# Kernel tuning notes

Measured on AMD Instinct MI355X. Metric: run time of the kernel, lower is better.

Reference implementation:

```python
import jax, jax.numpy as jnp
import numpy as np

B, S, H, GRID = 8, 4096, 1152, 64  # 64x64 patch grid, pooled 4x4 -> 256


def setup_inputs() -> dict:
    key = jax.random.key(0)
    k1, = jax.random.split(key, 1)
    hidden_states = jax.random.normal(k1, (B, S, H), dtype=jnp.float32)
    idx = jnp.arange(S, dtype=jnp.int32)
    pos = jnp.stack([idx % GRID, idx // GRID], axis=-1)  # (S,2) = (x,y)
    pixel_position_ids = jnp.broadcast_to(pos, (B, S, 2))
    padding_positions = jnp.zeros((B, S), dtype=bool)
    return {
        "hidden_states": hidden_states,
        "pixel_position_ids": pixel_position_ids,
        "padding_positions": padding_positions,
        "output_length": 256,
    }


def reference(hidden_states, pixel_position_ids, padding_positions, output_length):
    # 1) zero out padding rows
    hs = jnp.where(padding_positions[..., None], 0.0, hidden_states)
    hidden_size = hs.shape[-1]
    seq_len = hs.shape[1]
    k = int((seq_len // output_length) ** 0.5)
    k_sq = k * k
    assert k_sq * output_length == seq_len
    # 2) position-indexed 2D average pool via one-hot matmul
    clamped = jnp.clip(pixel_position_ids, 0).astype(jnp.int32)
    max_x = jnp.max(clamped[..., 0], axis=-1, keepdims=True) + 1  # [B,1]
    kern = clamped // k
    kernel_idxs = kern[..., 0] + (max_x // k) * kern[..., 1]  # [B,S]
    weights = jax.nn.one_hot(kernel_idxs, output_length, dtype=jnp.float32) / k_sq  # [B,S,L]
    pooled = jnp.einsum('bsl,bsh->blh', weights, hs.astype(jnp.float32)).astype(hs.dtype)
    pooler_mask = jnp.any(weights != 0, axis=1)  # [B,L]
    # 3) scale by sqrt(hidden_size)
    pooled = pooled * (hidden_size ** 0.5)
    return pooled, pooler_mask
```

## Files before the change

kernel.cpp:

```cpp
#include <hip/hip_runtime.h>
#include <math.h>

#define BB   8
#define SS   4096
#define HH   1152
#define LL   256
#define KP   4
#define KSQ  16
#define CAP  32
#define H4   (HH / 4)
#define TPB  256
#define I4   (SS / (2 * TPB))

typedef float f32x4 __attribute__((ext_vector_type(4)));

__global__ __launch_bounds__(TPB) void fused_pool_kernel(
    const float* __restrict__ hs,
    const int* __restrict__ pos,
    const unsigned char* __restrict__ pad,
    float* __restrict__ out)
{
    const int bl = blockIdx.x;
    const int b  = bl >> 8;
    const int l  = bl & (LL - 1);
    const int t  = threadIdx.x;

    const int x0 = (l & 15) * KP;
    const int y0 = (l >> 4) * KP;

    const unsigned char* pb = pad + (size_t)b * SS;
    const int4*  p4 = (const int4*)(pos + (size_t)b * SS * 2);
    const f32x4* hb = (const f32x4*)hs + (size_t)b * SS * H4;
    const bool has2 = t < (H4 - TPB);

    unsigned int pw[4];
#pragma unroll
    for (int g = 0; g < 4; ++g)
        pw[g] = *(const unsigned int*)(pb + (y0 + g) * 64 + x0);

    bool ok = true;
    f32x4 a0 = {0.f, 0.f, 0.f, 0.f};
    f32x4 a1 = {0.f, 0.f, 0.f, 0.f};

#pragma unroll
    for (int g = 0; g < 4; ++g) {
        const int4 u0 = p4[t + TPB * (2 * g)];
        const int4 u1 = p4[t + TPB * (2 * g + 1)];

        const int sbase = (y0 + g) * 64 + x0;
#pragma unroll
        for (int r = 0; r < 4; ++r) {
            const f32x4* row = hb + (size_t)(sbase + r) * H4;
            const float w = ((pw[g] >> (8 * r)) & 0xffu) ? 0.f : 1.f;
            a0 += w * row[t];
            if (has2) a1 += w * row[t + TPB];
        }

        const int s0 = 2 * (t + TPB * (2 * g));
        ok = ok && (u0.x == (s0 & 63)) && (u0.y == (s0 >> 6))
                && (u0.z == ((s0 + 1) & 63)) && (u0.w == ((s0 + 1) >> 6));
        const int s1 = 2 * (t + TPB * (2 * g + 1));
        ok = ok && (u1.x == (s1 & 63)) && (u1.y == (s1 >> 6))
                && (u1.z == ((s1 + 1) & 63)) && (u1.w == ((s1 + 1) >> 6));
    }

    __shared__ int s_wok[TPB / 64];
    __shared__ int s_wmax[TPB / 64];
    __shared__ int s_cnt;
    __shared__ int s_list[CAP];
    const bool wok = __all(ok);
    if ((t & 63) == 0) s_wok[t >> 6] = wok ? 1 : 0;
    if (t == 0) s_cnt = 0;
    __syncthreads();

    const float scale = sqrtf((float)HH) / (float)KSQ;

    if (s_wok[0] & s_wok[1] & s_wok[2] & s_wok[3]) {
        a0 *= scale; a1 *= scale;
        f32x4* orow = (f32x4*)out + (size_t)bl * H4;
        orow[t] = a0;
        if (has2) orow[t + TPB] = a1;
        if (t == 0) out[(size_t)BB * LL * HH + bl] = 1.0f;
        return;
    }

    int mx = 0;
    int4 v[I4];
#pragma unroll
    for (int i = 0; i < I4; ++i) {
        v[i] = p4[t + TPB * i];
        mx = max(mx, max(max(v[i].x, v[i].z), 0));
    }
#pragma unroll
    for (int off = 32; off >= 1; off >>= 1)
        mx = max(mx, __shfl_xor(mx, off));
    if ((t & 63) == 0) s_wmax[t >> 6] = mx;
    __syncthreads();
    const int m = max(max(s_wmax[0], s_wmax[1]), max(s_wmax[2], s_wmax[3]));
    const int stride = (m + 1) / KP;

#pragma unroll
    for (int i = 0; i < I4; ++i) {
        const int s0 = 2 * (t + TPB * i);
        {
            const int x = max(v[i].x, 0), y = max(v[i].y, 0);
            const int ki = x / KP + stride * (y / KP);
            if (ki == l) {
                const int slot = atomicAdd(&s_cnt, 1);
                if (slot < CAP) s_list[slot] = pb[s0] ? -1 : s0;
            }
        }
        {
            const int s1 = s0 + 1;
            const int x = max(v[i].z, 0), y = max(v[i].w, 0);
            const int ki = x / KP + stride * (y / KP);
            if (ki == l) {
                const int slot = atomicAdd(&s_cnt, 1);
                if (slot < CAP) s_list[slot] = pb[s1] ? -1 : s1;
            }
        }
    }
    __syncthreads();

    const int c  = s_cnt;
    const int cc = min(c, CAP);
    f32x4 b0 = {0.f, 0.f, 0.f, 0.f};
    f32x4 b1 = {0.f, 0.f, 0.f, 0.f};
    for (int i = 0; i < cc; ++i) {
        const int s = s_list[i];
        if (s < 0) continue;
        const f32x4* row = hb + (size_t)s * H4;
        b0 += row[t];
        if (has2) b1 += row[t + TPB];
    }
    b0 *= scale; b1 *= scale;
    f32x4* orow = (f32x4*)out + (size_t)bl * H4;
    orow[t] = b0;
    if (has2) orow[t + TPB] = b1;
    if (t == 0)
        out[(size_t)BB * LL * HH + bl] = (c > 0) ? 1.0f : 0.0f;
}

extern "C" void kernel_launch(void* const* d_in, const int* in_sizes, int n_in,
                              void* d_out, int out_size, void* d_ws, size_t ws_size,
                              hipStream_t stream) {
    const float* hs          = (const float*)d_in[0];
    const int*   pos         = (const int*)d_in[1];
    const unsigned char* pad = (const unsigned char*)d_in[2];

    fused_pool_kernel<<<BB * LL, TPB, 0, stream>>>(hs, pos, pad, (float*)d_out);
}
```

Measured before the change: 36.49 us.

## Hoist position-id verification into a separate small pre-pass kernel

Before this change, every one of the 2048 pool blocks re-read the full 32KB position array of its batch to check that the ids follow the canonical grid layout. The check now runs once in a 64-block verify kernel that writes per-chunk verdicts to workspace. The pool kernel reads eight ints and takes the fast path. This removes redundant position loads and the block-wide sync from the fast path, at the cost of an extra kernel launch and a dependency between the two kernels.

```diff
diff --git a/kernel.cpp b/kernel.cpp
--- a/kernel.cpp
+++ b/kernel.cpp
@@ -11,13 +11,37 @@
 #define H4   (HH / 4)
 #define TPB  256
 #define I4   (SS / (2 * TPB))
+#define NVER 64
 
 typedef float f32x4 __attribute__((ext_vector_type(4)));
 
-__global__ __launch_bounds__(TPB) void fused_pool_kernel(
+__global__ __launch_bounds__(TPB) void verify_kernel(
+    const int* __restrict__ pos,
+    int* __restrict__ verdict)
+{
+    const int v = blockIdx.x;
+    const int b = v >> 3;
+    const int q = v & 7;
+    const int t = threadIdx.x;
+
+    const int4 u = ((const int4*)pos)[(size_t)b * (SS / 2) + q * 256 + t];
+    const int s0 = q * 512 + 2 * t;
+    bool ok = (u.x == (s0 & 63)) && (u.y == (s0 >> 6))
+           && (u.z == ((s0 + 1) & 63)) && (u.w == ((s0 + 1) >> 6));
+
+    __shared__ int s_wok[TPB / 64];
+    const bool wok = __all(ok);
+    if ((t & 63) == 0) s_wok[t >> 6] = wok ? 1 : 0;
+    __syncthreads();
+    if (t == 0)
+        verdict[v] = s_wok[0] & s_wok[1] & s_wok[2] & s_wok[3];
+}
+
+__global__ __launch_bounds__(TPB) void pool_kernel(
     const float* __restrict__ hs,
     const int* __restrict__ pos,
     const unsigned char* __restrict__ pad,
+    const int* __restrict__ verdict,
     float* __restrict__ out)
 {
     const int bl = blockIdx.x;
@@ -29,53 +53,34 @@
     const int y0 = (l >> 4) * KP;
 
     const unsigned char* pb = pad + (size_t)b * SS;
-    const int4*  p4 = (const int4*)(pos + (size_t)b * SS * 2);
     const f32x4* hb = (const f32x4*)hs + (size_t)b * SS * H4;
     const bool has2 = t < (H4 - TPB);
-
-    unsigned int pw[4];
-#pragma unroll
-    for (int g = 0; g < 4; ++g)
-        pw[g] = *(const unsigned int*)(pb + (y0 + g) * 64 + x0);
-
-    bool ok = true;
-    f32x4 a0 = {0.f, 0.f, 0.f, 0.f};
-    f32x4 a1 = {0.f, 0.f, 0.f, 0.f};
-
-#pragma unroll
-    for (int g = 0; g < 4; ++g) {
-        const int4 u0 = p4[t + TPB * (2 * g)];
-        const int4 u1 = p4[t + TPB * (2 * g + 1)];
-
-        const int sbase = (y0 + g) * 64 + x0;
-#pragma unroll
-        for (int r = 0; r < 4; ++r) {
-            const f32x4* row = hb + (size_t)(sbase + r) * H4;
-            const float w = ((pw[g] >> (8 * r)) & 0xffu) ? 0.f : 1.f;
-            a0 += w * row[t];
-            if (has2) a1 += w * row[t + TPB];
-        }
-
-        const int s0 = 2 * (t + TPB * (2 * g));
-        ok = ok && (u0.x == (s0 & 63)) && (u0.y == (s0 >> 6))
-                && (u0.z == ((s0 + 1) & 63)) && (u0.w == ((s0 + 1) >> 6));
-        const int s1 = 2 * (t + TPB * (2 * g + 1));
-        ok = ok && (u1.x == (s1 & 63)) && (u1.y == (s1 >> 6))
-                && (u1.z == ((s1 + 1) & 63)) && (u1.w == ((s1 + 1) >> 6));
-    }
-
-    __shared__ int s_wok[TPB / 64];
-    __shared__ int s_wmax[TPB / 64];
-    __shared__ int s_cnt;
-    __shared__ int s_list[CAP];
-    const bool wok = __all(ok);
-    if ((t & 63) == 0) s_wok[t >> 6] = wok ? 1 : 0;
-    if (t == 0) s_cnt = 0;
-    __syncthreads();
-
     const float scale = sqrtf((float)HH) / (float)KSQ;
 
-    if (s_wok[0] & s_wok[1] & s_wok[2] & s_wok[3]) {
+    const int4 w0 = ((const int4*)verdict)[b * 2];
+    const int4 w1 = ((const int4*)verdict)[b * 2 + 1];
+    const bool idok = w0.x && w0.y && w0.z && w0.w &&
+                      w1.x && w1.y && w1.z && w1.w;
+
+    if (idok) {
+        unsigned int pw[4];
+#pragma unroll
+        for (int g = 0; g < 4; ++g)
+            pw[g] = *(const unsigned int*)(pb + (y0 + g) * 64 + x0);
+
+        f32x4 a0 = {0.f, 0.f, 0.f, 0.f};
+        f32x4 a1 = {0.f, 0.f, 0.f, 0.f};
+#pragma unroll
+        for (int g = 0; g < 4; ++g) {
+            const int sbase = (y0 + g) * 64 + x0;
+#pragma unroll
+            for (int r = 0; r < 4; ++r) {
+                const f32x4* row = hb + (size_t)(sbase + r) * H4;
+                const float w = ((pw[g] >> (8 * r)) & 0xffu) ? 0.f : 1.f;
+                a0 += w * row[t];
+                if (has2) a1 += w * row[t + TPB];
+            }
+        }
         a0 *= scale; a1 *= scale;
         f32x4* orow = (f32x4*)out + (size_t)bl * H4;
         orow[t] = a0;
@@ -84,6 +89,12 @@
         return;
     }
 
+    __shared__ int s_wmax[TPB / 64];
+    __shared__ int s_cnt;
+    __shared__ int s_list[CAP];
+    if (t == 0) s_cnt = 0;
+
+    const int4* p4 = (const int4*)(pos + (size_t)b * SS * 2);
     int mx = 0;
     int4 v[I4];
 #pragma unroll
@@ -148,5 +159,9 @@
     const int*   pos         = (const int*)d_in[1];
     const unsigned char* pad = (const unsigned char*)d_in[2];
 
-    fused_pool_kernel<<<BB * LL, TPB, 0, stream>>>(hs, pos, pad, (float*)d_out);
+    int* verdict = (int*)d_ws;
+
+    verify_kernel<<<NVER, TPB, 0, stream>>>(pos, verdict);
+    pool_kernel<<<BB * LL, TPB, 0, stream>>>(hs, pos, pad, verdict,
+                                             (float*)d_out);
 }
```

After: 34.21 us. -6.3%, faster.
